# Kernel optimization log

Hardware: AMD Instinct MI355X
Metric: run time of the kernel (lower is better)

The kernel has to match this reference:

```python
import jax, jax.numpy as jnp
import numpy as np

# Tree layout: NUM_LEVELS topological levels, M nodes per level; children of a node in
# level l are drawn from levels < l (level-0 nodes are leaves). This batches all
# independent same-level nodes, exactly the structure the per-node python loop implies.
NUM_LEVELS = 16
N_NODES = 16384
M_PER_LEVEL = N_NODES // NUM_LEVELS  # 1024
K_CHILD = 4
D_IN = 1024
D_HID = 256


def _linear_params(key, fan_in, fan_out):
    kw, kb = jax.random.split(key)
    bound = 1.0 / np.sqrt(fan_in)
    W = jax.random.uniform(kw, (fan_out, fan_in), jnp.float32, -bound, bound)
    b = jax.random.uniform(kb, (fan_out,), jnp.float32, -bound, bound)
    return W, b


def setup_inputs() -> dict:
    key = jax.random.key(0)
    kx, k1, k2, k3, k4 = jax.random.split(key, 5)
    x = jax.random.normal(kx, (N_NODES, D_IN), dtype=jnp.float32)

    # children: [N, K] int32, -1 = no child; child indices lie in strictly lower levels
    rng = np.random.default_rng(0)
    level = np.arange(N_NODES) // M_PER_LEVEL  # [N]
    lo_count = np.maximum(level * M_PER_LEVEL, 1)  # nodes available below each node
    cand = (rng.random((N_NODES, K_CHILD)) * lo_count[:, None]).astype(np.int64)
    present = (rng.random((N_NODES, K_CHILD)) < 0.6) & (level[:, None] > 0)
    children = jnp.asarray(np.where(present, cand, -1), dtype=jnp.int32)

    Wioux, bioux = _linear_params(k1, D_IN, 3 * D_HID)
    Wiouh, biouh = _linear_params(k2, D_HID, 3 * D_HID)
    Wfx, bfx = _linear_params(k3, D_IN, D_HID)
    Wfh, bfh = _linear_params(k4, D_HID, D_HID)
    return {"x": x, "children": children,
            "Wioux": Wioux, "bioux": bioux, "Wiouh": Wiouh, "biouh": biouh,
            "Wfx": Wfx, "bfx": bfx, "Wfh": Wfh, "bfh": bfh}


def reference(x, children, Wioux, bioux, Wiouh, biouh, Wfx, bfx, Wfh, bfh):
    N, _ = x.shape
    H = Wfh.shape[0]
    K = children.shape[1]
    L = NUM_LEVELS
    M = N // L

    # Input-dependent gate pre-activations: one big GEMM for all nodes (ioux / fx)
    iou_x = (x @ Wioux.T + bioux).reshape(L, M, 3 * H)
    f_x = (x @ Wfx.T + bfx).reshape(L, M, H)
    ch = jnp.maximum(children, 0).reshape(L, M, K)
    mk = (children >= 0).astype(x.dtype).reshape(L, M, K)

    def step(carry, inp):
        h, c = carry  # [N, H] each
        l, iou_xl, f_xl, chl, ml = inp
        h_ch = h[chl] * ml[..., None]  # [M, K, H] gathered child hidden states
        c_ch = c[chl] * ml[..., None]  # [M, K, H]
        # child-sum TreeLSTM: i/o/u gates use sum of child hidden states
        iou = iou_xl + h_ch.sum(axis=1) @ Wiouh.T + biouh  # [M, 3H]
        ig, og, ug = jnp.split(iou, 3, axis=-1)
        ig, og, ug = jax.nn.sigmoid(ig), jax.nn.sigmoid(og), jnp.tanh(ug)
        # per-child forget gates
        f = jax.nn.sigmoid(f_xl[:, None, :] + h_ch @ Wfh.T + bfh)  # [M, K, H]
        cl = ig * ug + jnp.sum(f * c_ch, axis=1)  # [M, H]
        hl = og * jnp.tanh(cl)
        h = jax.lax.dynamic_update_slice(h, hl, (l * M, 0))
        c = jax.lax.dynamic_update_slice(c, cl, (l * M, 0))
        return (h, c), None

    init = (jnp.zeros((N, H), x.dtype), jnp.zeros((N, H), x.dtype))
    xs = (jnp.arange(L, dtype=jnp.int32), iou_x, f_x, ch, mk)
    (h, _), _ = jax.lax.scan(step, init, xs)
    return h  # [N, H] hidden state of every node
```

## Files before the change

### kernel.cpp

```cpp
#include <hip/hip_runtime.h>
#include <stdint.h>

typedef __attribute__((ext_vector_type(8))) short bf16x8;
typedef __attribute__((ext_vector_type(4))) float f32x4;
typedef __attribute__((ext_vector_type(4))) unsigned int u32x4;
typedef unsigned short u16;
typedef unsigned int u32;

#define NLVL 16
#define NNODE 16384
#define DIN 1024
#define DH 256

__device__ __forceinline__ u16 f2bf(float f) {
  u32 u = __builtin_bit_cast(u32, f);
  u += 0x7FFFu + ((u >> 16) & 1u);
  return (u16)(u >> 16);
}
__device__ __forceinline__ float b2f(u16 h) {
  u32 u = ((u32)h) << 16;
  return __builtin_bit_cast(float, u);
}
__device__ __forceinline__ float fsig(float x) {
  return __builtin_amdgcn_rcpf(1.0f + __expf(-x));
}
__device__ __forceinline__ float ftanh(float x) {
  return 1.0f - 2.0f * __builtin_amdgcn_rcpf(__expf(2.0f * x) + 1.0f);
}

__device__ __forceinline__ void async_copy16(const void* g, void* lds) {
  __builtin_amdgcn_global_load_lds((const __attribute__((address_space(1))) void*)g,
                                   (__attribute__((address_space(3))) void*)lds, 16, 0, 0);
}

__device__ __forceinline__ void gload_x4(u32x4& v, const void* p) {
  asm volatile("global_load_dwordx4 %0, %1, off sc0 sc1" : "=&v"(v) : "v"(p));
}
__device__ __forceinline__ u32x4 gload_x4_sync(const void* p) {
  u32x4 v;
  asm volatile("global_load_dwordx4 %0, %1, off sc0 sc1\n\ts_waitcnt vmcnt(0)"
               : "=&v"(v) : "v"(p) : "memory");
  return v;
}
__device__ __forceinline__ void gstore_dw(float* p, float v) {
  asm volatile("global_store_dword %0, %1, off sc0 sc1" :: "v"(p), "v"(v) : "memory");
}
__device__ __forceinline__ void gstore_sh(u16* p, u16 v) {
  u32 w = v;
  asm volatile("global_store_short %0, %1, off sc0 sc1" :: "v"(p), "v"(w) : "memory");
}
__device__ __forceinline__ float aload_f(const float* p) {
  u32 v = __hip_atomic_load((const u32*)p, __ATOMIC_RELAXED, __HIP_MEMORY_SCOPE_AGENT);
  return __builtin_bit_cast(float, v);
}

__global__ __launch_bounds__(256) void k_prep(
    const float* __restrict__ x,
    const float* __restrict__ Wioux, const float* __restrict__ Wfx,
    const float* __restrict__ Wiouh, const float* __restrict__ Wfh,
    const float* __restrict__ bioux, const float* __restrict__ bfx,
    const float* __restrict__ biouh, const float* __restrict__ bfh,
    u16* __restrict__ xb, u16* __restrict__ Wxb, u16* __restrict__ Whb,
    float* __restrict__ b1, float* __restrict__ b2, u32* __restrict__ flags) {
  if (blockIdx.x == 8833) {
    uint4* p = (uint4*)flags;
#pragma unroll
    for (int i = 0; i < 5; ++i)
      p[threadIdx.x + i * 256] = make_uint4(0u, 0u, 0u, 0u);
    return;
  }
  if (blockIdx.x < 8192) {
    size_t i = (size_t)blockIdx.x * 256 + threadIdx.x;
    const float4* p = (const float4*)x + i * 2;
    float4 v0 = p[0], v1 = p[1];
    union { u16 s[8]; uint4 v; } o;
    o.s[0] = f2bf(v0.x); o.s[1] = f2bf(v0.y); o.s[2] = f2bf(v0.z); o.s[3] = f2bf(v0.w);
    o.s[4] = f2bf(v1.x); o.s[5] = f2bf(v1.y); o.s[6] = f2bf(v1.z); o.s[7] = f2bf(v1.w);
    *((uint4*)(xb + i * 8)) = o.v;
    return;
  }
  int t = (blockIdx.x - 8192) * 256 + threadIdx.x;
  if (t < 131072) {
    int idx = t * 8;
    int row = idx >> 10, col = idx & 1023;
    const float* src = (row < 768) ? (Wioux + (size_t)row * 1024 + col)
                                   : (Wfx + (size_t)(row - 768) * 1024 + col);
    union { u16 s[8]; uint4 v; } o;
#pragma unroll
    for (int j = 0; j < 8; ++j) o.s[j] = f2bf(src[j]);
    *((uint4*)(Wxb + idx)) = o.v;
  } else if (t < 163840) {
    int idx = (t - 131072) * 8;
    int row = idx >> 8, col = idx & 255;
    const float* src = (row < 768) ? (Wiouh + (size_t)row * 256 + col)
                                   : (Wfh + (size_t)(row - 768) * 256 + col);
    union { u16 s[8]; uint4 v; } o;
#pragma unroll
    for (int j = 0; j < 8; ++j) o.s[j] = f2bf(src[j]);
    *((uint4*)(Whb + idx)) = o.v;
  } else if (t < 164096) {
    int idx = (t - 163840) * 8;
#pragma unroll
    for (int j = 0; j < 8; ++j) {
      int i = idx + j;
      if (i < 1024) b1[i] = (i < 768) ? bioux[i] : bfx[i - 768];
      else { int k = i - 1024; b2[k] = (k < 768) ? biouh[k] : bfh[k - 768]; }
    }
  }
}

__device__ __forceinline__ int swz2(int row) { return (row & 3) ^ ((row >> 2) & 3); }

__global__ __launch_bounds__(256) void k_fused(
    const u16* __restrict__ xb, const int* __restrict__ children,
    const u16* __restrict__ Wxb, const u16* __restrict__ Whb,
    const float* __restrict__ b1, const float* __restrict__ b2,
    float* __restrict__ gx, u16* __restrict__ hb, float* __restrict__ cb,
    float* __restrict__ hout, u32* __restrict__ flags, u32* __restrict__ gxf) {
  __shared__ __align__(16) char smem[75264];
  const int tid = threadIdx.x, w = tid >> 6, l = tid & 63;
  const int bid = blockIdx.x;

  if (bid < 256) {
    u16* As = (u16*)smem;
    u16* Bs = (u16*)(smem + 16384);
    const int wm = w >> 1, wn = w & 1;
    for (int r = 0; r < 4; ++r) {
      const int job = bid + r * 256;
      const int level = job >> 6, sub = job & 63;
      const int tM = level * 1024 + (sub >> 3) * 128, tN = (sub & 7) * 128;

      f32x4 acc[4][4];
#pragma unroll
      for (int mt = 0; mt < 4; ++mt)
#pragma unroll
        for (int nt = 0; nt < 4; ++nt) acc[mt][nt] = (f32x4){0.f, 0.f, 0.f, 0.f};

      auto stage = [&](int buf, int t) {
        int k0 = t * 32;
#pragma unroll
        for (int i = 0; i < 2; ++i) {
          int seg = w * 2 + i;
          int row = seg * 16 + (l >> 2);
          int qg = (l & 3) ^ swz2(row);
          async_copy16(xb + (size_t)(tM + row) * 1024 + k0 + qg * 8,
                       &As[buf * 4096 + seg * 512]);
          async_copy16(Wxb + (size_t)(tN + row) * 1024 + k0 + qg * 8,
                       &Bs[buf * 4096 + seg * 512]);
        }
      };
      auto compute = [&](int buf) {
        bf16x8 a[4], b[4];
#pragma unroll
        for (int mt = 0; mt < 4; ++mt) {
          int row = wm * 64 + mt * 16 + (l & 15);
          int cs = (l >> 4) ^ swz2(row);
          a[mt] = *(const bf16x8*)&As[buf * 4096 + row * 32 + cs * 8];
        }
#pragma unroll
        for (int nt = 0; nt < 4; ++nt) {
          int row = wn * 64 + nt * 16 + (l & 15);
          int cs = (l >> 4) ^ swz2(row);
          b[nt] = *(const bf16x8*)&Bs[buf * 4096 + row * 32 + cs * 8];
        }
#pragma unroll
        for (int mt = 0; mt < 4; ++mt)
#pragma unroll
          for (int nt = 0; nt < 4; ++nt)
            acc[mt][nt] = __builtin_amdgcn_mfma_f32_16x16x32_bf16(a[mt], b[nt], acc[mt][nt], 0, 0, 0);
      };

      stage(0, 0);
      __syncthreads();
      int buf = 0;
      for (int t = 0; t < 32; ++t) {
        if (t + 1 < 32) stage(buf ^ 1, t + 1);
        compute(buf);
        __syncthreads();
        buf ^= 1;
      }

#pragma unroll
      for (int mt = 0; mt < 4; ++mt)
#pragma unroll
        for (int nt = 0; nt < 4; ++nt) {
          int col = tN + wn * 64 + nt * 16 + (l & 15);
          float bias = b1[col];
          int rbase = tM + wm * 64 + mt * 16 + (l >> 4) * 4;
#pragma unroll
          for (int rr = 0; rr < 4; ++rr)
            gstore_dw(gx + (size_t)(rbase + rr) * 1024 + col, acc[mt][nt][rr] + bias);
        }
      asm volatile("s_waitcnt vmcnt(0)" ::: "memory");
      __syncthreads();
      if (tid == 0) {
        int Nsub = sub & 7;
        __hip_atomic_store(gxf + ((level * 8 + (sub >> 3)) * 2 + (Nsub & 1)) * 4 + (Nsub >> 1),
                           1u, __ATOMIC_RELAXED, __HIP_MEMORY_SCOPE_AGENT);
      }
    }
    return;
  }

  int* chAll = (int*)smem;
  u16* hch = (u16*)(smem + 4096);
  u16* hsum = (u16*)(smem + 36864);
  float* c_lds = (float*)(smem + 45056);
  float* iouA = (float*)(smem + 62464);
  const int lb = bid - 256;
  const int ntile = lb & 63;
  const int cg = lb >> 6;
  const int h0 = cg * 64;

  bf16x8 w1[3][8];
  int colg_[3]; float b1g_[3];
#pragma unroll
  for (int i = 0; i < 3; ++i) {
    int tt = w * 3 + i;
    int s = tt >> 2, t = tt & 3;
    int colg = s * 256 + h0 + t * 16 + (l & 15);
    colg_[i] = colg;
    b1g_[i] = b2[colg];
    const u16* bp = Whb + (size_t)colg * 256 + (l >> 4) * 8;
#pragma unroll
    for (int ks = 0; ks < 8; ++ks) w1[i][ks] = *(const bf16x8*)(bp + ks * 32);
  }
  bf16x8 w2[4][8];
  float b2g_[4];
#pragma unroll
  for (int nt = 0; nt < 4; ++nt) {
    int hcol = h0 + nt * 16 + (l & 15);
    b2g_[nt] = b2[768 + hcol];
    const u16* bp = Whb + (size_t)(768 + hcol) * 256 + (l >> 4) * 8;
#pragma unroll
    for (int ks = 0; ks < 8; ++ks) w2[nt][ks] = *(const bf16x8*)(bp + ks * 32);
  }

#pragma unroll
  for (int k = 0; k < 4; ++k) {
    int id = tid + k * 256;
    chAll[id] = children[(size_t)(id >> 6) * 4096 + ntile * 64 + (id & 63)];
  }
  __syncthreads();

  for (int level = 0; level < NLVL; ++level) {
    const int node0 = level * 1024 + ntile * 16;
    const int* ch = chAll + level * 64;
    const int thr = (level - 1) << 10;

    if (level > 0 && tid < 64) {
      int child = ch[tid];
      if (child >= 0 && child < thr) {
        const u32* fp = flags + (size_t)(child >> 4) * 4;
        for (;;) {
          u32x4 fv = gload_x4_sync(fp);
          if ((fv[0] & fv[1] & fv[2] & fv[3]) != 0u) break;
          __builtin_amdgcn_s_sleep(2);
        }
      }
    }
    if (tid == 0) {
      const u32* gp = gxf + ((level * 8 + (ntile >> 3)) * 2 + (cg >> 1)) * 4;
      for (;;) {
        u32x4 fv = gload_x4_sync(gp);
        if ((fv[0] & fv[1] & fv[2] & fv[3]) != 0u) break;
        __builtin_amdgcn_s_sleep(2);
      }
    }
    __syncthreads();

    u32x4 hv[8]; int hc[8];
#pragma unroll
    for (int it = 0; it < 8; ++it) {
      int id = tid + it * 256;
      int row = id >> 5, q = id & 31;
      int child = ch[row]; hc[it] = child;
      hv[it] = (u32x4){0u, 0u, 0u, 0u};
      if (child >= 0 && child < thr)
        gload_x4(hv[it], hb + (size_t)child * 256 + q * 8);
    }
    u32x4 cv[4]; int cc[4];
#pragma unroll
    for (int it = 0; it < 4; ++it) {
      int id = tid + it * 256;
      int row = id >> 4, qq = id & 15;
      int child = ch[row]; cc[it] = child;
      cv[it] = (u32x4){0u, 0u, 0u, 0u};
      if (child >= 0 && child < thr)
        gload_x4(cv[it], cb + (size_t)child * 256 + h0 + qq * 4);
    }

    if (level > 0) {
      if (tid < 64) {
        int child = ch[tid];
        if (child >= thr) {
          const u32* fp = flags + (size_t)(child >> 4) * 4;
          for (;;) {
            u32x4 fv = gload_x4_sync(fp);
            if ((fv[0] & fv[1] & fv[2] & fv[3]) != 0u) break;
            __builtin_amdgcn_s_sleep(1);
          }
        }
      }
      __syncthreads();

#pragma unroll
      for (int it = 0; it < 8; ++it) {
        int id = tid + it * 256;
        int row = id >> 5, q = id & 31;
        if (hc[it] >= thr)
          gload_x4(hv[it], hb + (size_t)hc[it] * 256 + q * 8);
      }
#pragma unroll
      for (int it = 0; it < 4; ++it) {
        int id = tid + it * 256;
        int row = id >> 4, qq = id & 15;
        if (cc[it] >= thr)
          gload_x4(cv[it], cb + (size_t)cc[it] * 256 + h0 + qq * 4);
      }
    }

    asm volatile("s_waitcnt vmcnt(0)"
                 : "+v"(hv[0]), "+v"(hv[1]), "+v"(hv[2]), "+v"(hv[3]),
                   "+v"(hv[4]), "+v"(hv[5]), "+v"(hv[6]), "+v"(hv[7]),
                   "+v"(cv[0]), "+v"(cv[1]), "+v"(cv[2]), "+v"(cv[3]) :: "memory");
    __builtin_amdgcn_sched_barrier(0);
#pragma unroll
    for (int it = 0; it < 8; ++it) {
      int id = tid + it * 256;
      int row = id >> 5, q = id & 31;
      *(u32x4*)&hch[row * 256 + ((q ^ (row & 7)) * 8)] = hv[it];
    }
#pragma unroll
    for (int it = 0; it < 4; ++it) {
      int id = tid + it * 256;
      int row = id >> 4, qq = id & 15;
      *(u32x4*)&c_lds[row * 68 + qq * 4] = cv[it];
    }
    __syncthreads();

    float gxv[3][4], fxv[4];
#pragma unroll
    for (int i = 0; i < 3; ++i)
#pragma unroll
      for (int r = 0; r < 4; ++r)
        gxv[i][r] = aload_f(gx + (size_t)(node0 + (l >> 4) * 4 + r) * 1024 + colg_[i]);
    {
      const int node = node0 + w * 4 + (l >> 4);
#pragma unroll
      for (int nt = 0; nt < 4; ++nt)
        fxv[nt] = aload_f(gx + (size_t)node * 1024 + 768 + h0 + nt * 16 + (l & 15));
    }
#pragma unroll
    for (int it = 0; it < 2; ++it) {
      int id = tid + it * 256;
      int row = id >> 5, q = id & 31;
      float s[8] = {0.f, 0.f, 0.f, 0.f, 0.f, 0.f, 0.f, 0.f};
#pragma unroll
      for (int k = 0; k < 4; ++k) {
        int hr = row * 4 + k;
        bf16x8 v = *(const bf16x8*)&hch[hr * 256 + ((q ^ (hr & 7)) * 8)];
#pragma unroll
        for (int j = 0; j < 8; ++j) s[j] += b2f((u16)v[j]);
      }
      union { u16 us[8]; u32x4 v4; } o;
#pragma unroll
      for (int j = 0; j < 8; ++j) o.us[j] = f2bf(s[j]);
      *(u32x4*)&hsum[row * 256 + ((q ^ (row & 7)) * 8)] = o.v4;
    }
    __syncthreads();

    bf16x8 a1[8];
    {
      int arow = l & 15;
#pragma unroll
      for (int ks = 0; ks < 8; ++ks) {
        int chunk = ks * 4 + (l >> 4);
        a1[ks] = *(const bf16x8*)&hsum[arow * 256 + ((chunk ^ (arow & 7)) * 8)];
      }
    }
#pragma unroll
    for (int i = 0; i < 3; ++i) {
      int tt = w * 3 + i;
      int s = tt >> 2, t = tt & 3;
      f32x4 acc = (f32x4){0.f, 0.f, 0.f, 0.f};
#pragma unroll
      for (int ks = 0; ks < 8; ++ks)
        acc = __builtin_amdgcn_mfma_f32_16x16x32_bf16(a1[ks], w1[i][ks], acc, 0, 0, 0);
      float bias = b1g_[i];
#pragma unroll
      for (int r = 0; r < 4; ++r) {
        int nodeL = (l >> 4) * 4 + r;
        float v = acc[r] + gxv[i][r] + bias;
        iouA[nodeL * 196 + s * 64 + t * 16 + (l & 15)] = (s < 2) ? fsig(v) : ftanh(v);
      }
    }
    __syncthreads();

    bf16x8 a2[8];
    {
      int arow = w * 16 + (l & 15);
#pragma unroll
      for (int ks = 0; ks < 8; ++ks) {
        int chunk = ks * 4 + (l >> 4);
        a2[ks] = *(const bf16x8*)&hch[arow * 256 + ((chunk ^ (arow & 7)) * 8)];
      }
    }
    const int nodeL = w * 4 + (l >> 4);
    const int node = node0 + nodeL;
    float hn[4];
#pragma unroll
    for (int nt = 0; nt < 4; ++nt) {
      int hl = nt * 16 + (l & 15);
      int hcol = h0 + hl;
      f32x4 acc = (f32x4){0.f, 0.f, 0.f, 0.f};
#pragma unroll
      for (int ks = 0; ks < 8; ++ks)
        acc = __builtin_amdgcn_mfma_f32_16x16x32_bf16(a2[ks], w2[nt][ks], acc, 0, 0, 0);
      float fx = fxv[nt] + b2g_[nt];
      float fcsum = 0.f;
#pragma unroll
      for (int r = 0; r < 4; ++r)
        fcsum += fsig(fx + acc[r]) * c_lds[(nodeL * 4 + r) * 68 + hl];
      float ig = iouA[nodeL * 196 + hl];
      float og = iouA[nodeL * 196 + 64 + hl];
      float ug = iouA[nodeL * 196 + 128 + hl];
      float cnew = ig * ug + fcsum;
      float hnew = og * ftanh(cnew);
      hn[nt] = hnew;
      if (level + 1 < NLVL) {
        gstore_dw(cb + (size_t)node * 256 + hcol, cnew);
        gstore_sh(hb + (size_t)node * 256 + hcol, f2bf(hnew));
      }
    }
    if (level + 1 < NLVL) {
      asm volatile("s_waitcnt vmcnt(0)" ::: "memory");
      __syncthreads();
      if (tid == 0)
        __hip_atomic_store(flags + (size_t)((level << 6) + ntile) * 4 + cg, 1u,
                           __ATOMIC_RELAXED, __HIP_MEMORY_SCOPE_AGENT);
    }
#pragma unroll
    for (int nt = 0; nt < 4; ++nt)
      hout[(size_t)node * 256 + h0 + nt * 16 + (l & 15)] = hn[nt];
  }
}

extern "C" void kernel_launch(void* const* d_in, const int* in_sizes, int n_in,
                              void* d_out, int out_size, void* d_ws, size_t ws_size,
                              hipStream_t stream) {
  const float* x = (const float*)d_in[0];
  const int* children = (const int*)d_in[1];
  const float* Wioux = (const float*)d_in[2];
  const float* bioux = (const float*)d_in[3];
  const float* Wiouh = (const float*)d_in[4];
  const float* biouh = (const float*)d_in[5];
  const float* Wfx = (const float*)d_in[6];
  const float* bfx = (const float*)d_in[7];
  const float* Wfh = (const float*)d_in[8];
  const float* bfh = (const float*)d_in[9];

  char* ws = (char*)d_ws;
  u16* xb = (u16*)(ws + 0);
  float* gx = (float*)(ws + 33554432);
  u16* hb = (u16*)(ws + 100663296);
  float* cb = (float*)(ws + 109051904);
  u16* Wxb = (u16*)(ws + 125829120);
  u16* Whb = (u16*)(ws + 127926272);
  float* b1 = (float*)(ws + 128450560);
  float* b2 = (float*)(ws + 128454656);
  u32* flags = (u32*)(ws + 128458752);
  u32* gxf = (u32*)(ws + 128475136);
  float* hout = (float*)d_out;

  k_prep<<<8834, 256, 0, stream>>>(x, Wioux, Wfx, Wiouh, Wfh, bioux, bfx, biouh, bfh,
                                   xb, Wxb, Whb, b1, b2, flags);
  k_fused<<<512, 256, 0, stream>>>(xb, children, Wxb, Whb, b1, b2,
                                   gx, hb, cb, hout, flags, gxf);
}
```

Baseline: 209.4 us.

## Split child processing into ready and late phases, overlapping compute with waits

Each level now first gathers the children that are already finished (from earlier levels), runs the hsum and MFMA work and the partial forget-gate sums on them, then waits for same-level-minus-one children. After that wait it gathers only the late children into zeroed LDS and adds their contributions by linearity. The forget-gate MFMA is also remapped so each wave holds one 16-column weight slice across four node groups, which cuts w2 register use from 32 to 8 vectors. The intent is to hide the dependency-wait latency behind useful compute, at the cost of a second hsum and MFMA pass plus extra barriers and LDS writes.

```diff
diff --git a/kernel.cpp b/kernel.cpp
--- a/kernel.cpp
+++ b/kernel.cpp
@@ -211,6 +211,7 @@
   const int ntile = lb & 63;
   const int cg = lb >> 6;
   const int h0 = cg * 64;
+  const int hl = w * 16 + (l & 15);
 
   bf16x8 w1[3][8];
   int colg_[3]; float b1g_[3];
@@ -225,15 +226,12 @@
 #pragma unroll
     for (int ks = 0; ks < 8; ++ks) w1[i][ks] = *(const bf16x8*)(bp + ks * 32);
   }
-  bf16x8 w2[4][8];
-  float b2g_[4];
-#pragma unroll
-  for (int nt = 0; nt < 4; ++nt) {
-    int hcol = h0 + nt * 16 + (l & 15);
-    b2g_[nt] = b2[768 + hcol];
-    const u16* bp = Whb + (size_t)(768 + hcol) * 256 + (l >> 4) * 8;
-#pragma unroll
-    for (int ks = 0; ks < 8; ++ks) w2[nt][ks] = *(const bf16x8*)(bp + ks * 32);
+  bf16x8 w2[8];
+  const float b2gv = b2[768 + h0 + hl];
+  {
+    const u16* bp = Whb + (size_t)(768 + h0 + hl) * 256 + (l >> 4) * 8;
+#pragma unroll
+    for (int ks = 0; ks < 8; ++ks) w2[ks] = *(const bf16x8*)(bp + ks * 32);
   }
 
 #pragma unroll
@@ -269,25 +267,128 @@
     }
     __syncthreads();
 
-    u32x4 hv[8]; int hc[8];
+    float gxv[3][4];
+#pragma unroll
+    for (int i = 0; i < 3; ++i)
+#pragma unroll
+      for (int r = 0; r < 4; ++r)
+        gxv[i][r] = aload_f(gx + (size_t)(node0 + (l >> 4) * 4 + r) * 1024 + colg_[i]);
+    float fxv[4];
+#pragma unroll
+    for (int g = 0; g < 4; ++g)
+      fxv[g] = aload_f(gx + (size_t)(node0 + g * 4 + (l >> 4)) * 1024 + 768 + h0 + hl);
+
+    {
+      u32x4 hv[8]; int hc[8];
+#pragma unroll
+      for (int it = 0; it < 8; ++it) {
+        int id = tid + it * 256;
+        int row = id >> 5, q = id & 31;
+        int child = ch[row]; hc[it] = child;
+        hv[it] = (u32x4){0u, 0u, 0u, 0u};
+        if (child >= 0 && child < thr)
+          gload_x4(hv[it], hb + (size_t)child * 256 + q * 8);
+      }
+      u32x4 cv[4]; int cc[4];
+#pragma unroll
+      for (int it = 0; it < 4; ++it) {
+        int id = tid + it * 256;
+        int row = id >> 4, qq = id & 15;
+        int child = ch[row]; cc[it] = child;
+        cv[it] = (u32x4){0u, 0u, 0u, 0u};
+        if (child >= 0 && child < thr)
+          gload_x4(cv[it], cb + (size_t)child * 256 + h0 + qq * 4);
+      }
+      asm volatile("s_waitcnt vmcnt(0)"
+                   : "+v"(hv[0]), "+v"(hv[1]), "+v"(hv[2]), "+v"(hv[3]),
+                     "+v"(hv[4]), "+v"(hv[5]), "+v"(hv[6]), "+v"(hv[7]),
+                     "+v"(cv[0]), "+v"(cv[1]), "+v"(cv[2]), "+v"(cv[3]) :: "memory");
+      __builtin_amdgcn_sched_barrier(0);
+#pragma unroll
+      for (int it = 0; it < 8; ++it) {
+        int id = tid + it * 256;
+        int row = id >> 5, q = id & 31;
+        *(u32x4*)&hch[row * 256 + ((q ^ (row & 7)) * 8)] = hv[it];
+      }
+#pragma unroll
+      for (int it = 0; it < 4; ++it) {
+        int id = tid + it * 256;
+        int row = id >> 4, qq = id & 15;
+        *(u32x4*)&c_lds[row * 68 + qq * 4] = cv[it];
+      }
+    }
+    __syncthreads();
+
+#pragma unroll
+    for (int it = 0; it < 2; ++it) {
+      int id = tid + it * 256;
+      int row = id >> 5, q = id & 31;
+      float s[8] = {0.f, 0.f, 0.f, 0.f, 0.f, 0.f, 0.f, 0.f};
+#pragma unroll
+      for (int k = 0; k < 4; ++k) {
+        int hr = row * 4 + k;
+        bf16x8 v = *(const bf16x8*)&hch[hr * 256 + ((q ^ (hr & 7)) * 8)];
+#pragma unroll
+        for (int j = 0; j < 8; ++j) s[j] += b2f((u16)v[j]);
+      }
+      union { u16 us[8]; u32x4 v4; } o;
+#pragma unroll
+      for (int j = 0; j < 8; ++j) o.us[j] = f2bf(s[j]);
+      *(u32x4*)&hsum[row * 256 + ((q ^ (row & 7)) * 8)] = o.v4;
+    }
+    __syncthreads();
+
+    f32x4 acc1[3];
+    {
+      bf16x8 a1[8];
+      int arow = l & 15;
+#pragma unroll
+      for (int ks = 0; ks < 8; ++ks) {
+        int chunk = ks * 4 + (l >> 4);
+        a1[ks] = *(const bf16x8*)&hsum[arow * 256 + ((chunk ^ (arow & 7)) * 8)];
+      }
+#pragma unroll
+      for (int i = 0; i < 3; ++i) {
+        acc1[i] = (f32x4){0.f, 0.f, 0.f, 0.f};
+#pragma unroll
+        for (int ks = 0; ks < 8; ++ks)
+          acc1[i] = __builtin_amdgcn_mfma_f32_16x16x32_bf16(a1[ks], w1[i][ks], acc1[i], 0, 0, 0);
+      }
+    }
+    f32x4 acc2[4];
+#pragma unroll
+    for (int g = 0; g < 4; ++g) {
+      bf16x8 a2[8];
+      int arow = g * 16 + (l & 15);
+#pragma unroll
+      for (int ks = 0; ks < 8; ++ks) {
+        int chunk = ks * 4 + (l >> 4);
+        a2[ks] = *(const bf16x8*)&hch[arow * 256 + ((chunk ^ (arow & 7)) * 8)];
+      }
+      acc2[g] = (f32x4){0.f, 0.f, 0.f, 0.f};
+#pragma unroll
+      for (int ks = 0; ks < 8; ++ks)
+        acc2[g] = __builtin_amdgcn_mfma_f32_16x16x32_bf16(a2[ks], w2[ks], acc2[g], 0, 0, 0);
+    }
+    float fcs[4];
+#pragma unroll
+    for (int g = 0; g < 4; ++g) {
+      fcs[g] = 0.f;
+      int n = g * 4 + (l >> 4);
+#pragma unroll
+      for (int r = 0; r < 4; ++r) {
+        int c_ = ch[n * 4 + r];
+        if (c_ >= 0 && c_ < thr)
+          fcs[g] += fsig(fxv[g] + b2gv + acc2[g][r]) * c_lds[(n * 4 + r) * 68 + hl];
+      }
+    }
+    __syncthreads();
+
 #pragma unroll
     for (int it = 0; it < 8; ++it) {
       int id = tid + it * 256;
       int row = id >> 5, q = id & 31;
-      int child = ch[row]; hc[it] = child;
-      hv[it] = (u32x4){0u, 0u, 0u, 0u};
-      if (child >= 0 && child < thr)
-        gload_x4(hv[it], hb + (size_t)child * 256 + q * 8);
-    }
-    u32x4 cv[4]; int cc[4];
-#pragma unroll
-    for (int it = 0; it < 4; ++it) {
-      int id = tid + it * 256;
-      int row = id >> 4, qq = id & 15;
-      int child = ch[row]; cc[it] = child;
-      cv[it] = (u32x4){0u, 0u, 0u, 0u};
-      if (child >= 0 && child < thr)
-        gload_x4(cv[it], cb + (size_t)child * 256 + h0 + qq * 4);
+      *(u32x4*)&hch[row * 256 + ((q ^ (row & 7)) * 8)] = (u32x4){0u, 0u, 0u, 0u};
     }
 
     if (level > 0) {
@@ -304,133 +405,134 @@
       }
       __syncthreads();
 
-#pragma unroll
-      for (int it = 0; it < 8; ++it) {
+      {
+        u32x4 hv[8]; int hc[8];
+#pragma unroll
+        for (int it = 0; it < 8; ++it) {
+          int id = tid + it * 256;
+          int row = id >> 5, q = id & 31;
+          int child = ch[row]; hc[it] = child;
+          hv[it] = (u32x4){0u, 0u, 0u, 0u};
+          if (child >= thr)
+            gload_x4(hv[it], hb + (size_t)child * 256 + q * 8);
+        }
+        u32x4 cv[4]; int cc[4];
+#pragma unroll
+        for (int it = 0; it < 4; ++it) {
+          int id = tid + it * 256;
+          int row = id >> 4, qq = id & 15;
+          int child = ch[row]; cc[it] = child;
+          cv[it] = (u32x4){0u, 0u, 0u, 0u};
+          if (child >= thr)
+            gload_x4(cv[it], cb + (size_t)child * 256 + h0 + qq * 4);
+        }
+        asm volatile("s_waitcnt vmcnt(0)"
+                     : "+v"(hv[0]), "+v"(hv[1]), "+v"(hv[2]), "+v"(hv[3]),
+                       "+v"(hv[4]), "+v"(hv[5]), "+v"(hv[6]), "+v"(hv[7]),
+                       "+v"(cv[0]), "+v"(cv[1]), "+v"(cv[2]), "+v"(cv[3]) :: "memory");
+        __builtin_amdgcn_sched_barrier(0);
+#pragma unroll
+        for (int it = 0; it < 8; ++it) {
+          int id = tid + it * 256;
+          int row = id >> 5, q = id & 31;
+          if (hc[it] >= thr)
+            *(u32x4*)&hch[row * 256 + ((q ^ (row & 7)) * 8)] = hv[it];
+        }
+#pragma unroll
+        for (int it = 0; it < 4; ++it) {
+          int id = tid + it * 256;
+          int row = id >> 4, qq = id & 15;
+          if (cc[it] >= thr)
+            *(u32x4*)&c_lds[row * 68 + qq * 4] = cv[it];
+        }
+      }
+      __syncthreads();
+
+#pragma unroll
+      for (int it = 0; it < 2; ++it) {
         int id = tid + it * 256;
         int row = id >> 5, q = id & 31;
-        if (hc[it] >= thr)
-          gload_x4(hv[it], hb + (size_t)hc[it] * 256 + q * 8);
-      }
-#pragma unroll
-      for (int it = 0; it < 4; ++it) {
-        int id = tid + it * 256;
-        int row = id >> 4, qq = id & 15;
-        if (cc[it] >= thr)
-          gload_x4(cv[it], cb + (size_t)cc[it] * 256 + h0 + qq * 4);
-      }
-    }
-
-    asm volatile("s_waitcnt vmcnt(0)"
-                 : "+v"(hv[0]), "+v"(hv[1]), "+v"(hv[2]), "+v"(hv[3]),
-                   "+v"(hv[4]), "+v"(hv[5]), "+v"(hv[6]), "+v"(hv[7]),
-                   "+v"(cv[0]), "+v"(cv[1]), "+v"(cv[2]), "+v"(cv[3]) :: "memory");
-    __builtin_amdgcn_sched_barrier(0);
-#pragma unroll
-    for (int it = 0; it < 8; ++it) {
-      int id = tid + it * 256;
-      int row = id >> 5, q = id & 31;
-      *(u32x4*)&hch[row * 256 + ((q ^ (row & 7)) * 8)] = hv[it];
-    }
-#pragma unroll
-    for (int it = 0; it < 4; ++it) {
-      int id = tid + it * 256;
-      int row = id >> 4, qq = id & 15;
-      *(u32x4*)&c_lds[row * 68 + qq * 4] = cv[it];
-    }
-    __syncthreads();
-
-    float gxv[3][4], fxv[4];
-#pragma unroll
-    for (int i = 0; i < 3; ++i)
-#pragma unroll
-      for (int r = 0; r < 4; ++r)
-        gxv[i][r] = aload_f(gx + (size_t)(node0 + (l >> 4) * 4 + r) * 1024 + colg_[i]);
-    {
-      const int node = node0 + w * 4 + (l >> 4);
-#pragma unroll
-      for (int nt = 0; nt < 4; ++nt)
-        fxv[nt] = aload_f(gx + (size_t)node * 1024 + 768 + h0 + nt * 16 + (l & 15));
-    }
-#pragma unroll
-    for (int it = 0; it < 2; ++it) {
-      int id = tid + it * 256;
-      int row = id >> 5, q = id & 31;
-      float s[8] = {0.f, 0.f, 0.f, 0.f, 0.f, 0.f, 0.f, 0.f};
-#pragma unroll
-      for (int k = 0; k < 4; ++k) {
-        int hr = row * 4 + k;
-        bf16x8 v = *(const bf16x8*)&hch[hr * 256 + ((q ^ (hr & 7)) * 8)];
-#pragma unroll
-        for (int j = 0; j < 8; ++j) s[j] += b2f((u16)v[j]);
-      }
-      union { u16 us[8]; u32x4 v4; } o;
-#pragma unroll
-      for (int j = 0; j < 8; ++j) o.us[j] = f2bf(s[j]);
-      *(u32x4*)&hsum[row * 256 + ((q ^ (row & 7)) * 8)] = o.v4;
-    }
-    __syncthreads();
-
-    bf16x8 a1[8];
-    {
-      int arow = l & 15;
-#pragma unroll
-      for (int ks = 0; ks < 8; ++ks) {
-        int chunk = ks * 4 + (l >> 4);
-        a1[ks] = *(const bf16x8*)&hsum[arow * 256 + ((chunk ^ (arow & 7)) * 8)];
-      }
-    }
+        float s[8] = {0.f, 0.f, 0.f, 0.f, 0.f, 0.f, 0.f, 0.f};
+#pragma unroll
+        for (int k = 0; k < 4; ++k) {
+          int hr = row * 4 + k;
+          bf16x8 v = *(const bf16x8*)&hch[hr * 256 + ((q ^ (hr & 7)) * 8)];
+#pragma unroll
+          for (int j = 0; j < 8; ++j) s[j] += b2f((u16)v[j]);
+        }
+        union { u16 us[8]; u32x4 v4; } o;
+#pragma unroll
+        for (int j = 0; j < 8; ++j) o.us[j] = f2bf(s[j]);
+        *(u32x4*)&hsum[row * 256 + ((q ^ (row & 7)) * 8)] = o.v4;
+      }
+      __syncthreads();
+
+      {
+        bf16x8 a1[8];
+        int arow = l & 15;
+#pragma unroll
+        for (int ks = 0; ks < 8; ++ks) {
+          int chunk = ks * 4 + (l >> 4);
+          a1[ks] = *(const bf16x8*)&hsum[arow * 256 + ((chunk ^ (arow & 7)) * 8)];
+        }
+#pragma unroll
+        for (int i = 0; i < 3; ++i)
+#pragma unroll
+          for (int ks = 0; ks < 8; ++ks)
+            acc1[i] = __builtin_amdgcn_mfma_f32_16x16x32_bf16(a1[ks], w1[i][ks], acc1[i], 0, 0, 0);
+      }
+#pragma unroll
+      for (int g = 0; g < 4; ++g) {
+        bf16x8 a2[8];
+        int arow = g * 16 + (l & 15);
+#pragma unroll
+        for (int ks = 0; ks < 8; ++ks) {
+          int chunk = ks * 4 + (l >> 4);
+          a2[ks] = *(const bf16x8*)&hch[arow * 256 + ((chunk ^ (arow & 7)) * 8)];
+        }
+#pragma unroll
+        for (int ks = 0; ks < 8; ++ks)
+          acc2[g] = __builtin_amdgcn_mfma_f32_16x16x32_bf16(a2[ks], w2[ks], acc2[g], 0, 0, 0);
+      }
+#pragma unroll
+      for (int g = 0; g < 4; ++g) {
+        int n = g * 4 + (l >> 4);
+#pragma unroll
+        for (int r = 0; r < 4; ++r) {
+          int c_ = ch[n * 4 + r];
+          if (c_ >= thr)
+            fcs[g] += fsig(fxv[g] + b2gv + acc2[g][r]) * c_lds[(n * 4 + r) * 68 + hl];
+        }
+      }
+    }
+
 #pragma unroll
     for (int i = 0; i < 3; ++i) {
       int tt = w * 3 + i;
       int s = tt >> 2, t = tt & 3;
-      f32x4 acc = (f32x4){0.f, 0.f, 0.f, 0.f};
-#pragma unroll
-      for (int ks = 0; ks < 8; ++ks)
-        acc = __builtin_amdgcn_mfma_f32_16x16x32_bf16(a1[ks], w1[i][ks], acc, 0, 0, 0);
-      float bias = b1g_[i];
 #pragma unroll
       for (int r = 0; r < 4; ++r) {
         int nodeL = (l >> 4) * 4 + r;
-        float v = acc[r] + gxv[i][r] + bias;
+        float v = acc1[i][r] + gxv[i][r] + b1g_[i];
         iouA[nodeL * 196 + s * 64 + t * 16 + (l & 15)] = (s < 2) ? fsig(v) : ftanh(v);
       }
     }
     __syncthreads();
 
-    bf16x8 a2[8];
-    {
-      int arow = w * 16 + (l & 15);
-#pragma unroll
-      for (int ks = 0; ks < 8; ++ks) {
-        int chunk = ks * 4 + (l >> 4);
-        a2[ks] = *(const bf16x8*)&hch[arow * 256 + ((chunk ^ (arow & 7)) * 8)];
-      }
-    }
-    const int nodeL = w * 4 + (l >> 4);
-    const int node = node0 + nodeL;
     float hn[4];
 #pragma unroll
-    for (int nt = 0; nt < 4; ++nt) {
-      int hl = nt * 16 + (l & 15);
-      int hcol = h0 + hl;
-      f32x4 acc = (f32x4){0.f, 0.f, 0.f, 0.f};
-#pragma unroll
-      for (int ks = 0; ks < 8; ++ks)
-        acc = __builtin_amdgcn_mfma_f32_16x16x32_bf16(a2[ks], w2[nt][ks], acc, 0, 0, 0);
-      float fx = fxv[nt] + b2g_[nt];
-      float fcsum = 0.f;
-#pragma unroll
-      for (int r = 0; r < 4; ++r)
-        fcsum += fsig(fx + acc[r]) * c_lds[(nodeL * 4 + r) * 68 + hl];
-      float ig = iouA[nodeL * 196 + hl];
-      float og = iouA[nodeL * 196 + 64 + hl];
-      float ug = iouA[nodeL * 196 + 128 + hl];
-      float cnew = ig * ug + fcsum;
+    for (int g = 0; g < 4; ++g) {
+      int n = g * 4 + (l >> 4);
+      int node = node0 + n;
+      float ig = iouA[n * 196 + hl];
+      float og = iouA[n * 196 + 64 + hl];
+      float ug = iouA[n * 196 + 128 + hl];
+      float cnew = ig * ug + fcs[g];
       float hnew = og * ftanh(cnew);
-      hn[nt] = hnew;
+      hn[g] = hnew;
       if (level + 1 < NLVL) {
-        gstore_dw(cb + (size_t)node * 256 + hcol, cnew);
-        gstore_sh(hb + (size_t)node * 256 + hcol, f2bf(hnew));
+        gstore_dw(cb + (size_t)node * 256 + h0 + hl, cnew);
+        gstore_sh(hb + (size_t)node * 256 + h0 + hl, f2bf(hnew));
       }
     }
     if (level + 1 < NLVL) {
@@ -441,8 +543,8 @@
                            __ATOMIC_RELAXED, __HIP_MEMORY_SCOPE_AGENT);
     }
 #pragma unroll
-    for (int nt = 0; nt < 4; ++nt)
-      hout[(size_t)node * 256 + h0 + nt * 16 + (l & 15)] = hn[nt];
+    for (int g = 0; g < 4; ++g)
+      hout[(size_t)(node0 + g * 4 + (l >> 4)) * 256 + h0 + hl] = hn[g];
   }
 }
 
```

Result: slower. 255.8 us (+22.1%).
